# Optimization experiments

Hardware: AMD Instinct MI355X
Metric: run time of the kernel (lower is better)

Reference implementation:

```python
import jax, jax.numpy as jnp
import numpy as np

DIM = 1024
NH = 16        # query heads
NKV = 4        # kv heads
HD = 64        # head dim
GROUPS = NH // NKV
SPATIAL = 16
NZ = SPATIAL * SPATIAL  # 256 latent tokens with 2D structure
SOFT_CAP = 50.0
SCALE = HD ** -0.5
EPS = 1e-6


def rope_2d_cos_sin(nz, hd, spatial, dtype):
    # 2D RoPE: first half of head_dim encodes row position, second half column.
    pos = jnp.arange(nz)
    row = (pos // spatial).astype(jnp.float32)
    col = (pos % spatial).astype(jnp.float32)
    quarter = hd // 4
    inv_freq = 1.0 / (10000.0 ** (jnp.arange(quarter, dtype=jnp.float32) / quarter))
    f_row = row[:, None] * inv_freq[None, :]   # (nz, hd/4)
    f_col = col[:, None] * inv_freq[None, :]   # (nz, hd/4)
    emb = jnp.concatenate([f_row, f_col], axis=-1)      # (nz, hd/2)
    emb = jnp.concatenate([emb, emb], axis=-1)          # (nz, hd)
    return jnp.cos(emb).astype(dtype), jnp.sin(emb).astype(dtype)


def rotate_half(x):
    x1, x2 = jnp.split(x, 2, axis=-1)
    return jnp.concatenate([-x2, x1], axis=-1)


def apply_rotary(x, cos, sin):
    return x * cos + rotate_half(x) * sin


def rms_norm(x, w):
    # RMSNorm over head_dim with learned per-dim scale (QKNorm)
    return x * jax.lax.rsqrt(jnp.mean(x * x, axis=-1, keepdims=True) + EPS) * w


def setup_inputs() -> dict:
    key = jax.random.key(0)
    ks = jax.random.split(key, 7)
    B, T, S = 4, 16, 264
    x = jax.random.normal(ks[0], (B, T, S, DIM), dtype=jnp.float32)
    wq = jax.random.normal(ks[1], (NH * HD, DIM), dtype=jnp.float32) * 0.02
    wk = jax.random.normal(ks[2], (NKV * HD, DIM), dtype=jnp.float32) * 0.02
    wv = jax.random.normal(ks[3], (NKV * HD, DIM), dtype=jnp.float32) * 0.02
    wo = jax.random.normal(ks[4], (DIM, NH * HD), dtype=jnp.float32) * 0.02
    q_norm_w = jnp.ones((HD,), dtype=jnp.float32)
    k_norm_w = jnp.ones((HD,), dtype=jnp.float32)
    return {"x": x, "wq": wq, "wk": wk, "wv": wv, "wo": wo,
            "q_norm_w": q_norm_w, "k_norm_w": k_norm_w}


def reference(x, wq, wk, wv, wo, q_norm_w, k_norm_w):
    B, T, S, D = x.shape
    xf = x.reshape(B * T, S, D)
    # projections (torch Linear: y = x @ W.T)
    q = (xf @ wq.T).reshape(B * T, S, NH, HD).transpose(0, 2, 1, 3)   # (BT,NH,S,HD)
    k = (xf @ wk.T).reshape(B * T, S, NKV, HD).transpose(0, 2, 1, 3)  # (BT,NKV,S,HD)
    v = (xf @ wv.T).reshape(B * T, S, NKV, HD).transpose(0, 2, 1, 3)
    # QKNorm
    q = rms_norm(q, q_norm_w)
    k = rms_norm(k, k_norm_w)
    # partial 2D RoPE on latent tokens only
    cos, sin = rope_2d_cos_sin(NZ, HD, SPATIAL, q.dtype)
    cos = cos[None, None]  # (1,1,NZ,HD)
    sin = sin[None, None]
    q = jnp.concatenate([apply_rotary(q[:, :, :NZ], cos, sin), q[:, :, NZ:]], axis=2)
    k = jnp.concatenate([apply_rotary(k[:, :, :NZ], cos, sin), k[:, :, NZ:]], axis=2)
    # GQA: expand kv heads (repeat_interleave == jnp.repeat)
    k = jnp.repeat(k, GROUPS, axis=1)
    v = jnp.repeat(v, GROUPS, axis=1)
    # attention with soft cap
    attn = jnp.einsum("bhqd,bhkd->bhqk", q, k) * SCALE
    attn = SOFT_CAP * jnp.tanh(attn / SOFT_CAP)
    attn = jax.nn.softmax(attn, axis=-1)
    out = jnp.einsum("bhqk,bhkd->bhqd", attn, v)
    out = out.transpose(0, 2, 1, 3).reshape(B * T, S, NH * HD)
    out = out @ wo.T
    return out.reshape(B, T, S, D)
```

## Files before the change

kernel.cpp:

```cpp
#include <hip/hip_runtime.h>

typedef __bf16 bf16;
typedef __bf16 bf16x8 __attribute__((ext_vector_type(8)));
typedef float  f32x4  __attribute__((ext_vector_type(4)));

#define DIM   1024
#define NH    16
#define NKV   4
#define HD    64
#define SLEN  264
#define BTOT  64
#define MROWS (BTOT * SLEN)
#define NQKV  1536
#define NZ    256
#define VPAD  288

__device__ __forceinline__ void gl_lds16(const bf16* g, bf16* l) {
    __builtin_amdgcn_global_load_lds((__attribute__((address_space(1))) void*)(g),
                                     (__attribute__((address_space(3))) void*)(l),
                                     16, 0, 0);
}

__global__ void cvt_f32_bf16(const float* __restrict__ src, bf16* __restrict__ dst, int n) {
    int i = (blockIdx.x * 256 + threadIdx.x) * 4;
    if (i < n) {
        float4 v = *(const float4*)(src + i);
        dst[i + 0] = (bf16)v.x; dst[i + 1] = (bf16)v.y;
        dst[i + 2] = (bf16)v.z; dst[i + 3] = (bf16)v.w;
    }
}

__global__ void cvt_wcat(const float* __restrict__ wq, const float* __restrict__ wk,
                         const float* __restrict__ wv, bf16* __restrict__ dst) {
    int i = (blockIdx.x * 256 + threadIdx.x) * 4;
    const float* src; int off;
    if (i < 1024 * 1024)      { src = wq; off = i; }
    else if (i < 1280 * 1024) { src = wk; off = i - 1024 * 1024; }
    else                      { src = wv; off = i - 1280 * 1024; }
    float4 v = *(const float4*)(src + off);
    dst[i + 0] = (bf16)v.x; dst[i + 1] = (bf16)v.y;
    dst[i + 2] = (bf16)v.z; dst[i + 3] = (bf16)v.w;
}

__global__ void rope_tab_kernel(float2* __restrict__ ctab) {
    int i = blockIdx.x * 256 + threadIdx.x;
    int s = i >> 5, d = i & 31;
    const float LN1 = 0.5756462732485115f;
    float pos = (d < 16) ? (float)(s >> 4) : (float)(s & 15);
    float ang = pos * expf(-(float)(d & 15) * LN1);
    float sn, cs; sincosf(ang, &sn, &cs);
    ctab[i] = make_float2(cs, sn);
}

#define GEMM_STAGE_PTRS(Mptr, tileRow, K, P)                                   \
    const bf16* P[4];                                                          \
    {                                                                          \
        _Pragma("unroll")                                                      \
        for (int k = 0; k < 4; k++) {                                          \
            int s = k * 256 + tid;                                             \
            int r = s >> 3, cp = s & 7;                                        \
            int c = cp ^ (r & 7);                                              \
            P[k] = (Mptr) + (size_t)((tileRow) + r) * (K) + c * 8;             \
        }                                                                      \
    }

__device__ __forceinline__ int swz(int row, int chunk) {
    return row * 64 + ((chunk ^ (row & 7)) * 8);
}

__global__ __launch_bounds__(256) void gemm_qkv(const bf16* __restrict__ A,
                                                const bf16* __restrict__ Bw,
                                                bf16* __restrict__ out,
                                                const float* __restrict__ qw,
                                                const float* __restrict__ kw,
                                                const float2* __restrict__ ctab) {
    __shared__ __align__(16) bf16 As[128 * 64];
    __shared__ __align__(16) bf16 Bs[128 * 64];
    const int tid  = threadIdx.x;
    const int wid  = tid >> 6, lane = tid & 63;
    const int quad = lane >> 4, r16 = lane & 15;
    const int bid = blockIdx.x;
    const int g = bid / 48, rr = bid - g * 48;
    const int bm = g * 4 + (rr & 3), bn = rr >> 2;
    const int wm = wid & 1, wn = wid >> 1;

    GEMM_STAGE_PTRS(A,  bm * 128, DIM, Ap)
    GEMM_STAGE_PTRS(Bw, bn * 128, DIM, Bp)

    f32x4 acc[4][4];
#pragma unroll
    for (int i = 0; i < 4; i++)
#pragma unroll
        for (int j = 0; j < 4; j++) acc[i][j] = (f32x4){0.f, 0.f, 0.f, 0.f};

    for (int k0 = 0; k0 < DIM; k0 += 64) {
        __syncthreads();
#pragma unroll
        for (int k = 0; k < 4; k++) {
            gl_lds16(Ap[k] + k0, As + (k * 256 + wid * 64) * 8);
            gl_lds16(Bp[k] + k0, Bs + (k * 256 + wid * 64) * 8);
        }
        __syncthreads();
#pragma unroll
        for (int ks = 0; ks < 2; ks++) {
            bf16x8 a[4], b[4];
#pragma unroll
            for (int i = 0; i < 4; i++) {
                a[i] = *(const bf16x8*)&As[swz(wm * 64 + i * 16 + r16, ks * 4 + quad)];
                b[i] = *(const bf16x8*)&Bs[swz(wn * 64 + i * 16 + r16, ks * 4 + quad)];
            }
#pragma unroll
            for (int i = 0; i < 4; i++)
#pragma unroll
                for (int j = 0; j < 4; j++)
                    acc[i][j] = __builtin_amdgcn_mfma_f32_16x16x32_bf16(a[i], b[j], acc[i][j], 0, 0, 0);
        }
    }

    const int colbase = bn * 128 + wn * 64;
    const int rowbase = bm * 128 + wm * 64;
    if (bn < 10) {
        const float* w = (bn < 8) ? qw : kw;
        float wreg[4];
#pragma unroll
        for (int j = 0; j < 4; j++) wreg[j] = w[j * 16 + r16];
#pragma unroll
        for (int i = 0; i < 4; i++)
#pragma unroll
            for (int r = 0; r < 4; r++) {
                float ss = 0.f;
#pragma unroll
                for (int j = 0; j < 4; j++) ss += acc[i][j][r] * acc[i][j][r];
                ss += __shfl_xor(ss, 1, 64);
                ss += __shfl_xor(ss, 2, 64);
                ss += __shfl_xor(ss, 4, 64);
                ss += __shfl_xor(ss, 8, 64);
                float rms = rsqrtf(ss * (1.f / 64.f) + 1e-6f);
                float xv[4];
#pragma unroll
                for (int j = 0; j < 4; j++) xv[j] = acc[i][j][r] * rms * wreg[j];
                int gm = rowbase + i * 16 + quad * 4 + r;
                int s = gm % SLEN;
                if (s < NZ) {
                    float2 cs0 = ctab[s * 32 + r16];
                    float2 cs1 = ctab[s * 32 + 16 + r16];
                    float a0 = xv[0] * cs0.x - xv[2] * cs0.y;
                    float a2 = xv[2] * cs0.x + xv[0] * cs0.y;
                    float a1 = xv[1] * cs1.x - xv[3] * cs1.y;
                    float a3 = xv[3] * cs1.x + xv[1] * cs1.y;
                    xv[0] = a0; xv[1] = a1; xv[2] = a2; xv[3] = a3;
                }
                size_t rowoff = (size_t)gm * NQKV + colbase + r16;
#pragma unroll
                for (int j = 0; j < 4; j++) out[rowoff + j * 16] = (bf16)xv[j];
            }
    } else {
#pragma unroll
        for (int i = 0; i < 4; i++)
#pragma unroll
            for (int j = 0; j < 4; j++)
#pragma unroll
                for (int r = 0; r < 4; r++) {
                    int gm = rowbase + i * 16 + quad * 4 + r;
                    int gn = colbase + j * 16 + r16;
                    out[(size_t)gm * NQKV + gn] = (bf16)acc[i][j][r];
                }
    }
}

__global__ __launch_bounds__(256) void gemm_bt(const bf16* __restrict__ A,
                                               const bf16* __restrict__ Bw,
                                               float* __restrict__ Cout) {
    __shared__ __align__(16) bf16 As[128 * 64];
    __shared__ __align__(16) bf16 Bs[128 * 64];
    const int tid  = threadIdx.x;
    const int wid  = tid >> 6, lane = tid & 63;
    const int quad = lane >> 4, r16 = lane & 15;
    const int bid = blockIdx.x;
    const int g = bid / 32, rr = bid - g * 32;
    const int bm = g * 4 + (rr & 3), bn = rr >> 2;
    const int wm = wid & 1, wn = wid >> 1;

    GEMM_STAGE_PTRS(A,  bm * 128, DIM, Ap)
    GEMM_STAGE_PTRS(Bw, bn * 128, DIM, Bp)

    f32x4 acc[4][4];
#pragma unroll
    for (int i = 0; i < 4; i++)
#pragma unroll
        for (int j = 0; j < 4; j++) acc[i][j] = (f32x4){0.f, 0.f, 0.f, 0.f};

    for (int k0 = 0; k0 < DIM; k0 += 64) {
        __syncthreads();
#pragma unroll
        for (int k = 0; k < 4; k++) {
            gl_lds16(Ap[k] + k0, As + (k * 256 + wid * 64) * 8);
            gl_lds16(Bp[k] + k0, Bs + (k * 256 + wid * 64) * 8);
        }
        __syncthreads();
#pragma unroll
        for (int ks = 0; ks < 2; ks++) {
            bf16x8 a[4], b[4];
#pragma unroll
            for (int i = 0; i < 4; i++) {
                a[i] = *(const bf16x8*)&As[swz(wm * 64 + i * 16 + r16, ks * 4 + quad)];
                b[i] = *(const bf16x8*)&Bs[swz(wn * 64 + i * 16 + r16, ks * 4 + quad)];
            }
#pragma unroll
            for (int i = 0; i < 4; i++)
#pragma unroll
                for (int j = 0; j < 4; j++)
                    acc[i][j] = __builtin_amdgcn_mfma_f32_16x16x32_bf16(a[i], b[j], acc[i][j], 0, 0, 0);
        }
    }

#pragma unroll
    for (int i = 0; i < 4; i++)
#pragma unroll
        for (int j = 0; j < 4; j++)
#pragma unroll
            for (int r = 0; r < 4; r++) {
                int gm = bm * 128 + wm * 64 + i * 16 + quad * 4 + r;
                int gn = bn * 128 + wn * 64 + j * 16 + r16;
                Cout[(size_t)gm * DIM + gn] = acc[i][j][r];
            }
}

__global__ __launch_bounds__(256) void vtrans_kernel(const bf16* __restrict__ qkv,
                                                     bf16* __restrict__ vt) {
    __shared__ bf16 Ls[64 * 272];
    const int tid = threadIdx.x;
    const int b = blockIdx.x, bt = b >> 2, kv = b & 3;
    const int part = tid >> 5;
    const int rr   = tid & 31;
#pragma unroll
    for (int pass = 0; pass < 9; ++pass) {
        int row = pass * 32 + rr;
        if (row < SLEN) {
            bf16x8 v = *(const bf16x8*)(qkv + (size_t)(bt * SLEN + row) * NQKV + 1280 + kv * 64 + part * 8);
#pragma unroll
            for (int j = 0; j < 8; j++) Ls[(part * 8 + j) * 272 + row] = v[j];
        }
    }
    __syncthreads();
    const int d = tid >> 2, seg = tid & 3;
    size_t obase = ((size_t)b * 64 + d) * VPAD;
#pragma unroll
    for (int m = 0; m < 9; ++m) {
        int col = seg * 72 + m * 8;
        bf16x8 o;
#pragma unroll
        for (int j = 0; j < 8; j++) {
            int s = col + j;
            o[j] = (s < SLEN) ? Ls[d * 272 + s] : (bf16)0.f;
        }
        *(bf16x8*)(vt + obase + col) = o;
    }
}

__global__ __launch_bounds__(256) void attn_kernel(const bf16* __restrict__ qkv,
                                                   const bf16* __restrict__ vt,
                                                   bf16* __restrict__ aout) {
    const int PLD = 40;
    __shared__ __align__(16) bf16 Pb[4][2][16 * PLD];

    const int tid = threadIdx.x;
    const int wid = tid >> 6, lane = tid & 63;
    const int quad = lane >> 4, r16 = lane & 15;
    const int qp = blockIdx.x;
    const int kv = blockIdx.y, bt = blockIdx.z;
    const int h = kv * 4 + wid;

    bf16x8 qa[2][2];
#pragma unroll
    for (int qi = 0; qi < 2; qi++) {
        int q0 = qp * 32 + qi * 16 + r16;
        int qcl = q0 < SLEN ? q0 : SLEN - 1;
        const bf16* qb = qkv + (size_t)(bt * SLEN + qcl) * NQKV + h * HD + quad * 8;
        qa[qi][0] = *(const bf16x8*)qb;
        qa[qi][1] = *(const bf16x8*)(qb + 32);
    }

    f32x4 oacc[2][4];
    float lsum[2][4];
#pragma unroll
    for (int qi = 0; qi < 2; qi++)
#pragma unroll
        for (int i = 0; i < 4; i++) { oacc[qi][i] = (f32x4){0.f, 0.f, 0.f, 0.f}; lsum[qi][i] = 0.f; }

    const bf16* kbase = qkv + (size_t)bt * SLEN * NQKV + 1024 + kv * HD + quad * 8;
    const bf16* vbase = vt + (size_t)(bt * 4 + kv) * HD * VPAD;

    bf16x8 nk[2][2];
#pragma unroll
    for (int kt = 0; kt < 2; kt++) {
        int key = kt * 16 + r16;
        const bf16* kp = kbase + (size_t)key * NQKV;
        nk[kt][0] = *(const bf16x8*)kp;
        nk[kt][1] = *(const bf16x8*)(kp + 32);
    }

    for (int c = 0; c < 9; ++c) {
        bf16x8 ck[2][2];
#pragma unroll
        for (int kt = 0; kt < 2; kt++) { ck[kt][0] = nk[kt][0]; ck[kt][1] = nk[kt][1]; }
        if (c < 8) {
#pragma unroll
            for (int kt = 0; kt < 2; kt++) {
                int key = (c + 1) * 32 + kt * 16 + r16;
                int kc = key < SLEN ? key : SLEN - 1;
                const bf16* kp = kbase + (size_t)kc * NQKV;
                nk[kt][0] = *(const bf16x8*)kp;
                nk[kt][1] = *(const bf16x8*)(kp + 32);
            }
        }
        bf16x8 cv[4];
#pragma unroll
        for (int dt = 0; dt < 4; ++dt)
            cv[dt] = *(const bf16x8*)(vbase + (size_t)(dt * 16 + r16) * VPAD + c * 32 + quad * 8);

        f32x4 s[2][2];
#pragma unroll
        for (int qi = 0; qi < 2; qi++)
#pragma unroll
            for (int kt = 0; kt < 2; kt++) {
                f32x4 t = (f32x4){0.f, 0.f, 0.f, 0.f};
                t = __builtin_amdgcn_mfma_f32_16x16x32_bf16(qa[qi][0], ck[kt][0], t, 0, 0, 0);
                t = __builtin_amdgcn_mfma_f32_16x16x32_bf16(qa[qi][1], ck[kt][1], t, 0, 0, 0);
                s[qi][kt] = t;
            }

#pragma unroll
        for (int qi = 0; qi < 2; qi++) {
            bf16* Pw = &Pb[wid][qi][0];
#pragma unroll
            for (int kt = 0; kt < 2; kt++)
#pragma unroll
                for (int r = 0; r < 4; ++r) {
                    int key = c * 32 + kt * 16 + r16;
                    float sc = s[qi][kt][r];
                    float z = sc * 0.0025f;
                    float z2 = z * z;
                    float poly = fmaf(z2, fmaf(z2, 0.133333333f, -0.333333333f), 1.f);
                    float p = exp2f(sc * 0.18033688f * poly);
                    p = (key < SLEN) ? p : 0.f;
                    bf16 pb = (bf16)p;
                    lsum[qi][r] += (float)pb;
                    Pw[(quad * 4 + r) * PLD + kt * 16 + r16] = pb;
                }
            bf16x8 pa = *(const bf16x8*)&Pw[r16 * PLD + quad * 8];
#pragma unroll
            for (int dt = 0; dt < 4; ++dt)
                oacc[qi][dt] = __builtin_amdgcn_mfma_f32_16x16x32_bf16(pa, cv[dt], oacc[qi][dt], 0, 0, 0);
        }
    }

#pragma unroll
    for (int qi = 0; qi < 2; qi++)
#pragma unroll
        for (int r = 0; r < 4; ++r) {
            float l = lsum[qi][r];
            l += __shfl_xor(l, 1, 64);
            l += __shfl_xor(l, 2, 64);
            l += __shfl_xor(l, 4, 64);
            l += __shfl_xor(l, 8, 64);
            float inv = 1.f / l;
            int q = qp * 32 + qi * 16 + quad * 4 + r;
            if (q < SLEN) {
                size_t base = (size_t)(bt * SLEN + q) * (NH * HD) + h * HD;
#pragma unroll
                for (int dt = 0; dt < 4; ++dt)
                    aout[base + dt * 16 + r16] = (bf16)(oacc[qi][dt][r] * inv);
            }
        }
}

extern "C" void kernel_launch(void* const* d_in, const int* in_sizes, int n_in,
                              void* d_out, int out_size, void* d_ws, size_t ws_size,
                              hipStream_t stream) {
    const float* x   = (const float*)d_in[0];
    const float* wq  = (const float*)d_in[1];
    const float* wk  = (const float*)d_in[2];
    const float* wv  = (const float*)d_in[3];
    const float* wo  = (const float*)d_in[4];
    const float* qnw = (const float*)d_in[5];
    const float* knw = (const float*)d_in[6];

    bf16* xbf  = (bf16*)d_ws;
    bf16* wcat = xbf  + (size_t)MROWS * DIM;
    bf16* wobf = wcat + (size_t)NQKV * DIM;
    bf16* qkv  = wobf + (size_t)DIM * DIM;
    bf16* vt   = qkv  + (size_t)MROWS * NQKV;
    float2* ctab = (float2*)(vt + (size_t)BTOT * NKV * HD * VPAD);
    bf16* aout = xbf;

    rope_tab_kernel<<<32, 256, 0, stream>>>(ctab);
    cvt_f32_bf16<<<(MROWS * DIM) / 1024, 256, 0, stream>>>(x, xbf, MROWS * DIM);
    cvt_wcat<<<(NQKV * DIM) / 1024, 256, 0, stream>>>(wq, wk, wv, wcat);
    cvt_f32_bf16<<<(DIM * DIM) / 1024, 256, 0, stream>>>(wo, wobf, DIM * DIM);

    gemm_qkv<<<(MROWS / 128) * (NQKV / 128), 256, 0, stream>>>(xbf, wcat, qkv, qnw, knw, ctab);
    vtrans_kernel<<<BTOT * NKV, 256, 0, stream>>>(qkv, vt);
    attn_kernel<<<dim3(9, NKV, BTOT), 256, 0, stream>>>(qkv, vt, aout);
    gemm_bt<<<(MROWS / 128) * (DIM / 128), 256, 0, stream>>>(aout, wobf, (float*)d_out);
}
```

Before: 351.6 us.

## Rewrite projection GEMMs as 256x256 tiles with multi-buffered LDS pipeline

Both projection GEMMs now use a shared 256x256-tile core with 512 threads (8 waves). It stages A and B into four LDS buffers each, with an interleaved prefetch schedule, vmcnt gating, raised wave priority around the MFMA blocks, and an XCD-aware workgroup remap. The aim is to overlap global-to-LDS loads with MFMA work and raise arithmetic intensity per tile, in place of the old single-buffer 128x128 loop that synchronised twice per K step. The cost is more LDS per block and hand-tuned barrier ordering, and correctness depends on 264-row sequences mapping onto 256-row tiles, which the QKNorm/RoPE epilogue handles per row.

```diff
diff --git a/kernel.cpp b/kernel.cpp
--- a/kernel.cpp
+++ b/kernel.cpp
@@ -52,177 +52,209 @@
     ctab[i] = make_float2(cs, sn);
 }
 
-#define GEMM_STAGE_PTRS(Mptr, tileRow, K, P)                                   \
-    const bf16* P[4];                                                          \
-    {                                                                          \
-        _Pragma("unroll")                                                      \
-        for (int k = 0; k < 4; k++) {                                          \
-            int s = k * 256 + tid;                                             \
-            int r = s >> 3, cp = s & 7;                                        \
-            int c = cp ^ (r & 7);                                              \
-            P[k] = (Mptr) + (size_t)((tileRow) + r) * (K) + c * 8;             \
-        }                                                                      \
-    }
-
-__device__ __forceinline__ int swz(int row, int chunk) {
-    return row * 64 + ((chunk ^ (row & 7)) * 8);
-}
-
-__global__ __launch_bounds__(256) void gemm_qkv(const bf16* __restrict__ A,
+
+#define GATE4  asm volatile("s_waitcnt vmcnt(4)" ::: "memory")
+#define NOGATE do {} while (0)
+
+#define STAGE_A(DST, H, KT) do {                                                       \
+    gl_lds16(Ag + (size_t)((H) * 128 + ars[0]) * DIM + (KT) * 64 + acs[0] * 8,         \
+             (DST) + (wid * 64) * 8);                                                  \
+    gl_lds16(Ag + (size_t)((H) * 128 + ars[1]) * DIM + (KT) * 64 + acs[1] * 8,         \
+             (DST) + (512 + wid * 64) * 8);                                            \
+} while (0)
+
+#define STAGE_B(DST, KS, KT) do {                                                      \
+    gl_lds16(Bg + (size_t)brs[0] * DIM + (KT) * 64 + (KS) * 32 + bcs[0] * 8,           \
+             (DST) + (wid * 64) * 8);                                                  \
+    gl_lds16(Bg + (size_t)brs[1] * DIM + (KT) * 64 + (KS) * 32 + bcs[1] * 8,           \
+             (DST) + (512 + wid * 64) * 8);                                            \
+} while (0)
+
+#define PHASE(AARR, BARR, AA, KS, STAGE_STMT, GATE_STMT) do {                          \
+    const bf16* Ab_ = (AARR) + aRdBase + axor[KS];                                     \
+    const bf16* Bb_ = (BARR) + bRdBase + bxorv;                                        \
+    bf16x8 af_[4], bf_[4];                                                             \
+    _Pragma("unroll")                                                                  \
+    for (int i_ = 0; i_ < 4; i_++) af_[i_] = *(const bf16x8*)(Ab_ + i_ * 1024);        \
+    _Pragma("unroll")                                                                  \
+    for (int n_ = 0; n_ < 4; n_++) bf_[n_] = *(const bf16x8*)(Bb_ + n_ * 512);         \
+    STAGE_STMT;                                                                        \
+    GATE_STMT;                                                                         \
+    asm volatile("s_barrier" ::: "memory");                                            \
+    __builtin_amdgcn_s_setprio(1);                                                     \
+    _Pragma("unroll")                                                                  \
+    for (int i_ = 0; i_ < 4; i_++)                                                     \
+        _Pragma("unroll")                                                              \
+        for (int n_ = 0; n_ < 4; n_++)                                                 \
+            acc[AA][i_][n_] = __builtin_amdgcn_mfma_f32_16x16x32_bf16(                 \
+                af_[i_], bf_[n_], acc[AA][i_][n_], 0, 0, 0);                           \
+    __builtin_amdgcn_s_setprio(0);                                                     \
+    asm volatile("s_barrier" ::: "memory");                                            \
+} while (0)
+
+__device__ __forceinline__ void gemm256_core(const bf16* __restrict__ Ag,
+                                             const bf16* __restrict__ Bg,
+                                             f32x4 (&acc)[2][4][4]) {
+    __shared__ __align__(16) bf16 A00[128 * 64], A01[128 * 64], A10[128 * 64], A11[128 * 64];
+    __shared__ __align__(16) bf16 B00[256 * 32], B01[256 * 32], B10[256 * 32], B11[256 * 32];
+
+    const int tid  = threadIdx.x;
+    const int wid  = tid >> 6, lane = tid & 63;
+    const int quad = lane >> 4, r16 = lane & 15;
+    const int wm = wid & 1, wn = wid >> 1;
+
+    int ars[2], acs[2], brs[2], bcs[2];
+#pragma unroll
+    for (int k = 0; k < 2; k++) {
+        int s = k * 512 + tid;
+        ars[k] = s >> 3; acs[k] = (s & 7) ^ (ars[k] & 7);
+        brs[k] = s >> 2; bcs[k] = (s & 3) ^ (brs[k] & 3);
+    }
+    const int aRdBase = (wm * 64 + r16) * 64;
+    const int bRdBase = (wn * 64 + r16) * 32;
+    const int axor[2] = { (quad ^ (r16 & 7)) * 8, ((4 + quad) ^ (r16 & 7)) * 8 };
+    const int bxorv   = (quad ^ (r16 & 3)) * 8;
+
+    STAGE_A(A00, 0, 0); STAGE_A(A01, 1, 0);
+    STAGE_B(B00, 0, 0); STAGE_B(B01, 1, 0);
+    STAGE_A(A10, 0, 1); STAGE_B(B10, 0, 1);
+    GATE4;
+    asm volatile("s_barrier" ::: "memory");
+
+#pragma unroll 1
+    for (int it = 0; it < 8; ++it) {
+        const int t1 = 2 * it + 1;
+        int t2 = 2 * it + 2; if (t2 > 15) t2 = 15;
+        int t3 = 2 * it + 3; if (t3 > 15) t3 = 15;
+        PHASE(A00, B00, 0, 0, STAGE_A(A11, 1, t1), NOGATE);
+        PHASE(A00, B01, 0, 1, STAGE_B(B11, 1, t1), NOGATE);
+        PHASE(A01, B00, 1, 0, STAGE_A(A00, 0, t2), NOGATE);
+        PHASE(A01, B01, 1, 1, STAGE_B(B00, 0, t2), GATE4);
+        PHASE(A10, B10, 0, 0, STAGE_A(A01, 1, t2), NOGATE);
+        PHASE(A10, B11, 0, 1, STAGE_B(B01, 1, t2), NOGATE);
+        PHASE(A11, B10, 1, 0, STAGE_A(A10, 0, t3), NOGATE);
+        PHASE(A11, B11, 1, 1, STAGE_B(B10, 0, t3), GATE4);
+    }
+}
+
+__device__ __forceinline__ int xcd_swizzle(int orig, int nwg) {
+    int q = nwg >> 3, r = nwg & 7;
+    int xcd = orig & 7, lid = orig >> 3;
+    return (xcd < r ? xcd * (q + 1) : r * (q + 1) + (xcd - r) * q) + lid;
+}
+
+__global__ __launch_bounds__(512) void gemm_qkv(const bf16* __restrict__ A,
                                                 const bf16* __restrict__ Bw,
                                                 bf16* __restrict__ out,
                                                 const float* __restrict__ qw,
                                                 const float* __restrict__ kw,
                                                 const float2* __restrict__ ctab) {
-    __shared__ __align__(16) bf16 As[128 * 64];
-    __shared__ __align__(16) bf16 Bs[128 * 64];
+    const int nwg = (MROWS / 256) * (NQKV / 256);
+    int wg = xcd_swizzle(blockIdx.x, nwg);
+    const int bm = wg / 6, bn = wg - bm * 6;
+
+    f32x4 acc[2][4][4];
+#pragma unroll
+    for (int a = 0; a < 2; a++)
+#pragma unroll
+        for (int i = 0; i < 4; i++)
+#pragma unroll
+            for (int n = 0; n < 4; n++) acc[a][i][n] = (f32x4){0.f, 0.f, 0.f, 0.f};
+
+    gemm256_core(A + (size_t)bm * 256 * DIM, Bw + (size_t)bn * 256 * DIM, acc);
+
     const int tid  = threadIdx.x;
     const int wid  = tid >> 6, lane = tid & 63;
     const int quad = lane >> 4, r16 = lane & 15;
-    const int bid = blockIdx.x;
-    const int g = bid / 48, rr = bid - g * 48;
-    const int bm = g * 4 + (rr & 3), bn = rr >> 2;
     const int wm = wid & 1, wn = wid >> 1;
-
-    GEMM_STAGE_PTRS(A,  bm * 128, DIM, Ap)
-    GEMM_STAGE_PTRS(Bw, bn * 128, DIM, Bp)
-
-    f32x4 acc[4][4];
-#pragma unroll
-    for (int i = 0; i < 4; i++)
-#pragma unroll
-        for (int j = 0; j < 4; j++) acc[i][j] = (f32x4){0.f, 0.f, 0.f, 0.f};
-
-    for (int k0 = 0; k0 < DIM; k0 += 64) {
-        __syncthreads();
-#pragma unroll
-        for (int k = 0; k < 4; k++) {
-            gl_lds16(Ap[k] + k0, As + (k * 256 + wid * 64) * 8);
-            gl_lds16(Bp[k] + k0, Bs + (k * 256 + wid * 64) * 8);
-        }
-        __syncthreads();
-#pragma unroll
-        for (int ks = 0; ks < 2; ks++) {
-            bf16x8 a[4], b[4];
-#pragma unroll
-            for (int i = 0; i < 4; i++) {
-                a[i] = *(const bf16x8*)&As[swz(wm * 64 + i * 16 + r16, ks * 4 + quad)];
-                b[i] = *(const bf16x8*)&Bs[swz(wn * 64 + i * 16 + r16, ks * 4 + quad)];
-            }
+    const int colbase = bn * 256 + wn * 64;
+    const int rowb    = bm * 256 + wm * 64;
+
+    if (bn < 5) {
+        const float* w = (bn < 4) ? qw : kw;
+        float wreg[4];
+#pragma unroll
+        for (int n = 0; n < 4; n++) wreg[n] = w[n * 16 + r16];
+#pragma unroll
+        for (int a = 0; a < 2; a++)
 #pragma unroll
             for (int i = 0; i < 4; i++)
 #pragma unroll
-                for (int j = 0; j < 4; j++)
-                    acc[i][j] = __builtin_amdgcn_mfma_f32_16x16x32_bf16(a[i], b[j], acc[i][j], 0, 0, 0);
-        }
-    }
-
-    const int colbase = bn * 128 + wn * 64;
-    const int rowbase = bm * 128 + wm * 64;
-    if (bn < 10) {
-        const float* w = (bn < 8) ? qw : kw;
-        float wreg[4];
-#pragma unroll
-        for (int j = 0; j < 4; j++) wreg[j] = w[j * 16 + r16];
-#pragma unroll
-        for (int i = 0; i < 4; i++)
-#pragma unroll
-            for (int r = 0; r < 4; r++) {
-                float ss = 0.f;
-#pragma unroll
-                for (int j = 0; j < 4; j++) ss += acc[i][j][r] * acc[i][j][r];
-                ss += __shfl_xor(ss, 1, 64);
-                ss += __shfl_xor(ss, 2, 64);
-                ss += __shfl_xor(ss, 4, 64);
-                ss += __shfl_xor(ss, 8, 64);
-                float rms = rsqrtf(ss * (1.f / 64.f) + 1e-6f);
-                float xv[4];
-#pragma unroll
-                for (int j = 0; j < 4; j++) xv[j] = acc[i][j][r] * rms * wreg[j];
-                int gm = rowbase + i * 16 + quad * 4 + r;
-                int s = gm % SLEN;
-                if (s < NZ) {
-                    float2 cs0 = ctab[s * 32 + r16];
-                    float2 cs1 = ctab[s * 32 + 16 + r16];
-                    float a0 = xv[0] * cs0.x - xv[2] * cs0.y;
-                    float a2 = xv[2] * cs0.x + xv[0] * cs0.y;
-                    float a1 = xv[1] * cs1.x - xv[3] * cs1.y;
-                    float a3 = xv[3] * cs1.x + xv[1] * cs1.y;
-                    xv[0] = a0; xv[1] = a1; xv[2] = a2; xv[3] = a3;
+                for (int r = 0; r < 4; r++) {
+                    float ss = 0.f;
+#pragma unroll
+                    for (int n = 0; n < 4; n++) ss += acc[a][i][n][r] * acc[a][i][n][r];
+                    ss += __shfl_xor(ss, 1, 64);
+                    ss += __shfl_xor(ss, 2, 64);
+                    ss += __shfl_xor(ss, 4, 64);
+                    ss += __shfl_xor(ss, 8, 64);
+                    float rms = rsqrtf(ss * (1.f / 64.f) + 1e-6f);
+                    float xv[4];
+#pragma unroll
+                    for (int n = 0; n < 4; n++) xv[n] = acc[a][i][n][r] * rms * wreg[n];
+                    int gm = rowb + a * 128 + i * 16 + quad * 4 + r;
+                    int s = gm % SLEN;
+                    if (s < NZ) {
+                        float2 cs0 = ctab[s * 32 + r16];
+                        float2 cs1 = ctab[s * 32 + 16 + r16];
+                        float a0 = xv[0] * cs0.x - xv[2] * cs0.y;
+                        float a2 = xv[2] * cs0.x + xv[0] * cs0.y;
+                        float a1 = xv[1] * cs1.x - xv[3] * cs1.y;
+                        float a3 = xv[3] * cs1.x + xv[1] * cs1.y;
+                        xv[0] = a0; xv[1] = a1; xv[2] = a2; xv[3] = a3;
+                    }
+                    size_t rowoff = (size_t)gm * NQKV + colbase + r16;
+#pragma unroll
+                    for (int n = 0; n < 4; n++) out[rowoff + n * 16] = (bf16)xv[n];
                 }
-                size_t rowoff = (size_t)gm * NQKV + colbase + r16;
-#pragma unroll
-                for (int j = 0; j < 4; j++) out[rowoff + j * 16] = (bf16)xv[j];
-            }
     } else {
 #pragma unroll
-        for (int i = 0; i < 4; i++)
-#pragma unroll
-            for (int j = 0; j < 4; j++)
+        for (int a = 0; a < 2; a++)
+#pragma unroll
+            for (int i = 0; i < 4; i++)
 #pragma unroll
                 for (int r = 0; r < 4; r++) {
-                    int gm = rowbase + i * 16 + quad * 4 + r;
-                    int gn = colbase + j * 16 + r16;
-                    out[(size_t)gm * NQKV + gn] = (bf16)acc[i][j][r];
+                    int gm = rowb + a * 128 + i * 16 + quad * 4 + r;
+                    size_t rowoff = (size_t)gm * NQKV + colbase + r16;
+#pragma unroll
+                    for (int n = 0; n < 4; n++) out[rowoff + n * 16] = (bf16)acc[a][i][n][r];
                 }
     }
 }
 
-__global__ __launch_bounds__(256) void gemm_bt(const bf16* __restrict__ A,
+__global__ __launch_bounds__(512) void gemm_bt(const bf16* __restrict__ A,
                                                const bf16* __restrict__ Bw,
                                                float* __restrict__ Cout) {
-    __shared__ __align__(16) bf16 As[128 * 64];
-    __shared__ __align__(16) bf16 Bs[128 * 64];
+    const int nwg = (MROWS / 256) * (DIM / 256);
+    int wg = xcd_swizzle(blockIdx.x, nwg);
+    const int bm = wg / 4, bn = wg - bm * 4;
+
+    f32x4 acc[2][4][4];
+#pragma unroll
+    for (int a = 0; a < 2; a++)
+#pragma unroll
+        for (int i = 0; i < 4; i++)
+#pragma unroll
+            for (int n = 0; n < 4; n++) acc[a][i][n] = (f32x4){0.f, 0.f, 0.f, 0.f};
+
+    gemm256_core(A + (size_t)bm * 256 * DIM, Bw + (size_t)bn * 256 * DIM, acc);
+
     const int tid  = threadIdx.x;
     const int wid  = tid >> 6, lane = tid & 63;
     const int quad = lane >> 4, r16 = lane & 15;
-    const int bid = blockIdx.x;
-    const int g = bid / 32, rr = bid - g * 32;
-    const int bm = g * 4 + (rr & 3), bn = rr >> 2;
     const int wm = wid & 1, wn = wid >> 1;
-
-    GEMM_STAGE_PTRS(A,  bm * 128, DIM, Ap)
-    GEMM_STAGE_PTRS(Bw, bn * 128, DIM, Bp)
-
-    f32x4 acc[4][4];
-#pragma unroll
-    for (int i = 0; i < 4; i++)
-#pragma unroll
-        for (int j = 0; j < 4; j++) acc[i][j] = (f32x4){0.f, 0.f, 0.f, 0.f};
-
-    for (int k0 = 0; k0 < DIM; k0 += 64) {
-        __syncthreads();
-#pragma unroll
-        for (int k = 0; k < 4; k++) {
-            gl_lds16(Ap[k] + k0, As + (k * 256 + wid * 64) * 8);
-            gl_lds16(Bp[k] + k0, Bs + (k * 256 + wid * 64) * 8);
-        }
-        __syncthreads();
-#pragma unroll
-        for (int ks = 0; ks < 2; ks++) {
-            bf16x8 a[4], b[4];
-#pragma unroll
-            for (int i = 0; i < 4; i++) {
-                a[i] = *(const bf16x8*)&As[swz(wm * 64 + i * 16 + r16, ks * 4 + quad)];
-                b[i] = *(const bf16x8*)&Bs[swz(wn * 64 + i * 16 + r16, ks * 4 + quad)];
-            }
-#pragma unroll
-            for (int i = 0; i < 4; i++)
-#pragma unroll
-                for (int j = 0; j < 4; j++)
-                    acc[i][j] = __builtin_amdgcn_mfma_f32_16x16x32_bf16(a[i], b[j], acc[i][j], 0, 0, 0);
-        }
-    }
-
-#pragma unroll
-    for (int i = 0; i < 4; i++)
-#pragma unroll
-        for (int j = 0; j < 4; j++)
+    const int colbase = bn * 256 + wn * 64;
+    const int rowb    = bm * 256 + wm * 64;
+#pragma unroll
+    for (int a = 0; a < 2; a++)
+#pragma unroll
+        for (int i = 0; i < 4; i++)
 #pragma unroll
             for (int r = 0; r < 4; r++) {
-                int gm = bm * 128 + wm * 64 + i * 16 + quad * 4 + r;
-                int gn = bn * 128 + wn * 64 + j * 16 + r16;
-                Cout[(size_t)gm * DIM + gn] = acc[i][j][r];
+                int gm = rowb + a * 128 + i * 16 + quad * 4 + r;
+                size_t rowoff = (size_t)gm * DIM + colbase + r16;
+#pragma unroll
+                for (int n = 0; n < 4; n++) Cout[rowoff + n * 16] = acc[a][i][n][r];
             }
 }
 
@@ -399,8 +431,8 @@
     cvt_wcat<<<(NQKV * DIM) / 1024, 256, 0, stream>>>(wq, wk, wv, wcat);
     cvt_f32_bf16<<<(DIM * DIM) / 1024, 256, 0, stream>>>(wo, wobf, DIM * DIM);
 
-    gemm_qkv<<<(MROWS / 128) * (NQKV / 128), 256, 0, stream>>>(xbf, wcat, qkv, qnw, knw, ctab);
+    gemm_qkv<<<(MROWS / 256) * (NQKV / 256), 512, 0, stream>>>(xbf, wcat, qkv, qnw, knw, ctab);
     vtrans_kernel<<<BTOT * NKV, 256, 0, stream>>>(qkv, vt);
     attn_kernel<<<dim3(9, NKV, BTOT), 256, 0, stream>>>(qkv, vt, aout);
-    gemm_bt<<<(MROWS / 128) * (DIM / 128), 256, 0, stream>>>(aout, wobf, (float*)d_out);
-}
+    gemm_bt<<<(MROWS / 256) * (DIM / 256), 512, 0, stream>>>(aout, wobf, (float*)d_out);
+}
```

After: 372.0 us. +5.8%, slower.

## Rewrite QKV GEMM as 256x256 tile, 8-wave pipelined kernel with XCD swizzle

Applied to the files above, without the earlier changes.

Replaces the 128x128, 4-wave QKV projection GEMM with a 256x256 tile, 512-thread kernel. It double-buffers quarter tiles in LDS and overlaps global-to-LDS loads with MFMA phases through explicit vmcnt gating, barriers and setprio. Blocks are remapped so neighbouring tiles land on the same XCD, which should improve L2 reuse. The aim is higher MFMA utilisation and fewer sync stalls, at the cost of 128KB of LDS per block, only one block per CU, and a smaller grid (396 blocks), which may hurt load balance.

```diff
diff --git a/kernel.cpp b/kernel.cpp
--- a/kernel.cpp
+++ b/kernel.cpp
@@ -52,6 +52,170 @@
     ctab[i] = make_float2(cs, sn);
 }
 
+__device__ __forceinline__ int xcd_swizzle(int orig, int nwg) {
+    int q = nwg >> 3, r = nwg & 7;
+    int xcd = orig & 7, lid = orig >> 3;
+    return (xcd < r ? xcd * (q + 1) : r * (q + 1) + (xcd - r) * q) + lid;
+}
+
+
+#define GATE2  asm volatile("s_waitcnt vmcnt(2)" ::: "memory")
+#define NOGATE do {} while (0)
+
+#define STAGE(DST, G, H, KT) do {                                              \
+    gl_lds16((G) + (size_t)((H) * 128 + rs0) * DIM + (KT) * 64 + cs0 * 8,      \
+             (DST) + wid * 512);                                               \
+    gl_lds16((G) + (size_t)((H) * 128 + 64 + rs0) * DIM + (KT) * 64 + cs0 * 8, \
+             (DST) + 4096 + wid * 512);                                        \
+} while (0)
+
+#define PHASE(Ad, Bd, AA, KS, STAGE_STMT, GATE_STMT) do {                      \
+    bf16x8 af_[4], bf_[4];                                                     \
+    _Pragma("unroll")                                                          \
+    for (int i_ = 0; i_ < 4; i_++) {                                           \
+        af_[i_] = *(const bf16x8*)((Ad) + aRdBase + i_ * 1024 + xorv[KS]);     \
+        bf_[i_] = *(const bf16x8*)((Bd) + bRdBase + i_ * 1024 + xorv[KS]);     \
+    }                                                                          \
+    STAGE_STMT;                                                                \
+    GATE_STMT;                                                                 \
+    __builtin_amdgcn_s_barrier();                                              \
+    asm volatile("s_waitcnt lgkmcnt(0)" ::: "memory");                         \
+    __builtin_amdgcn_sched_barrier(0);                                         \
+    __builtin_amdgcn_s_setprio(1);                                             \
+    _Pragma("unroll")                                                          \
+    for (int i_ = 0; i_ < 4; i_++)                                             \
+        _Pragma("unroll")                                                      \
+        for (int n_ = 0; n_ < 4; n_++)                                         \
+            acc[AA][i_][n_] = __builtin_amdgcn_mfma_f32_16x16x32_bf16(         \
+                af_[i_], bf_[n_], acc[AA][i_][n_], 0, 0, 0);                   \
+    __builtin_amdgcn_s_setprio(0);                                             \
+    __builtin_amdgcn_s_barrier();                                              \
+} while (0)
+
+__device__ __forceinline__ void gemm256_core(const bf16* __restrict__ Ag,
+                                             const bf16* __restrict__ Bg,
+                                             f32x4 (&acc)[2][4][4]) {
+    __shared__ __align__(16) bf16 A00[128 * 64], A01[128 * 64], A10[128 * 64], A11[128 * 64];
+    __shared__ __align__(16) bf16 B00[128 * 64], B01[128 * 64], B10[128 * 64], B11[128 * 64];
+
+    const int tid  = threadIdx.x;
+    const int wid  = tid >> 6, lane = tid & 63;
+    const int quad = lane >> 4, r16 = lane & 15;
+    const int wm = wid & 1, wn = wid >> 1;
+
+    const int rs0 = tid >> 3;
+    const int cs0 = (tid & 7) ^ (rs0 & 7);
+
+    const int aRdBase = (wm * 64 + r16) * 64;
+    const int bRdBase = ((wn & 1) * 64 + r16) * 64;
+    const int xorv[2] = { (quad ^ (r16 & 7)) * 8, ((4 + quad) ^ (r16 & 7)) * 8 };
+
+    const bf16* Bd0 = (wn & 2) ? B01 : B00;
+    const bf16* Bd1 = (wn & 2) ? B11 : B10;
+
+    STAGE(A00, Ag, 0, 0);
+    STAGE(A01, Ag, 1, 0);
+    STAGE(B00, Bg, 0, 0);
+    STAGE(B01, Bg, 1, 0);
+    STAGE(A10, Ag, 0, 1);
+    GATE2;
+    __builtin_amdgcn_s_barrier();
+
+#pragma unroll 1
+    for (int it = 0; it < 8; ++it) {
+        const int t1 = 2 * it + 1;
+        int t2 = 2 * it + 2; if (t2 > 15) t2 = 15;
+        int t3 = 2 * it + 3; if (t3 > 15) t3 = 15;
+        PHASE(A00, Bd0, 0, 0, STAGE(A11, Ag, 1, t1), NOGATE);
+        PHASE(A00, Bd0, 0, 1, STAGE(B10, Bg, 0, t1), NOGATE);
+        PHASE(A01, Bd0, 1, 0, STAGE(B11, Bg, 1, t1), NOGATE);
+        PHASE(A01, Bd0, 1, 1, STAGE(A00, Ag, 0, t2), GATE2);
+        PHASE(A10, Bd1, 0, 0, STAGE(A01, Ag, 1, t2), NOGATE);
+        PHASE(A10, Bd1, 0, 1, STAGE(B00, Bg, 0, t2), NOGATE);
+        PHASE(A11, Bd1, 1, 0, STAGE(B01, Bg, 1, t2), NOGATE);
+        PHASE(A11, Bd1, 1, 1, STAGE(A10, Ag, 0, t3), GATE2);
+    }
+}
+
+__global__ __launch_bounds__(512) void gemm_qkv(const bf16* __restrict__ A,
+                                                const bf16* __restrict__ Bw,
+                                                bf16* __restrict__ out,
+                                                const float* __restrict__ qw,
+                                                const float* __restrict__ kw,
+                                                const float2* __restrict__ ctab) {
+    const int nwg = (MROWS / 256) * (NQKV / 256);
+    int wg = xcd_swizzle(blockIdx.x, nwg);
+    const int bm = wg / 6, bn = wg - bm * 6;
+
+    f32x4 acc[2][4][4];
+#pragma unroll
+    for (int a = 0; a < 2; a++)
+#pragma unroll
+        for (int i = 0; i < 4; i++)
+#pragma unroll
+            for (int n = 0; n < 4; n++) acc[a][i][n] = (f32x4){0.f, 0.f, 0.f, 0.f};
+
+    gemm256_core(A + (size_t)bm * 256 * DIM, Bw + (size_t)bn * 256 * DIM, acc);
+
+    const int tid  = threadIdx.x;
+    const int wid  = tid >> 6, lane = tid & 63;
+    const int quad = lane >> 4, r16 = lane & 15;
+    const int wm = wid & 1, wn = wid >> 1;
+    const int colbase = bn * 256 + wn * 64;
+    const int rowb    = bm * 256 + wm * 64;
+
+    if (bn < 5) {
+        const float* w = (bn < 4) ? qw : kw;
+        float wreg[4];
+#pragma unroll
+        for (int n = 0; n < 4; n++) wreg[n] = w[n * 16 + r16];
+#pragma unroll
+        for (int a = 0; a < 2; a++)
+#pragma unroll
+            for (int i = 0; i < 4; i++)
+#pragma unroll
+                for (int r = 0; r < 4; r++) {
+                    float ss = 0.f;
+#pragma unroll
+                    for (int n = 0; n < 4; n++) ss += acc[a][i][n][r] * acc[a][i][n][r];
+                    ss += __shfl_xor(ss, 1, 64);
+                    ss += __shfl_xor(ss, 2, 64);
+                    ss += __shfl_xor(ss, 4, 64);
+                    ss += __shfl_xor(ss, 8, 64);
+                    float rms = rsqrtf(ss * (1.f / 64.f) + 1e-6f);
+                    float xv[4];
+#pragma unroll
+                    for (int n = 0; n < 4; n++) xv[n] = acc[a][i][n][r] * rms * wreg[n];
+                    int gm = rowb + a * 128 + i * 16 + quad * 4 + r;
+                    int s = gm % SLEN;
+                    if (s < NZ) {
+                        float2 cs0 = ctab[s * 32 + r16];
+                        float2 cs1 = ctab[s * 32 + 16 + r16];
+                        float a0 = xv[0] * cs0.x - xv[2] * cs0.y;
+                        float a2 = xv[2] * cs0.x + xv[0] * cs0.y;
+                        float a1 = xv[1] * cs1.x - xv[3] * cs1.y;
+                        float a3 = xv[3] * cs1.x + xv[1] * cs1.y;
+                        xv[0] = a0; xv[1] = a1; xv[2] = a2; xv[3] = a3;
+                    }
+                    size_t rowoff = (size_t)gm * NQKV + colbase + r16;
+#pragma unroll
+                    for (int n = 0; n < 4; n++) out[rowoff + n * 16] = (bf16)xv[n];
+                }
+    } else {
+#pragma unroll
+        for (int a = 0; a < 2; a++)
+#pragma unroll
+            for (int i = 0; i < 4; i++)
+#pragma unroll
+                for (int r = 0; r < 4; r++) {
+                    int gm = rowb + a * 128 + i * 16 + quad * 4 + r;
+                    size_t rowoff = (size_t)gm * NQKV + colbase + r16;
+#pragma unroll
+                    for (int n = 0; n < 4; n++) out[rowoff + n * 16] = (bf16)acc[a][i][n][r];
+                }
+    }
+}
+
 #define GEMM_STAGE_PTRS(Mptr, tileRow, K, P)                                   \
     const bf16* P[4];                                                          \
     {                                                                          \
@@ -66,106 +230,6 @@
 
 __device__ __forceinline__ int swz(int row, int chunk) {
     return row * 64 + ((chunk ^ (row & 7)) * 8);
-}
-
-__global__ __launch_bounds__(256) void gemm_qkv(const bf16* __restrict__ A,
-                                                const bf16* __restrict__ Bw,
-                                                bf16* __restrict__ out,
-                                                const float* __restrict__ qw,
-                                                const float* __restrict__ kw,
-                                                const float2* __restrict__ ctab) {
-    __shared__ __align__(16) bf16 As[128 * 64];
-    __shared__ __align__(16) bf16 Bs[128 * 64];
-    const int tid  = threadIdx.x;
-    const int wid  = tid >> 6, lane = tid & 63;
-    const int quad = lane >> 4, r16 = lane & 15;
-    const int bid = blockIdx.x;
-    const int g = bid / 48, rr = bid - g * 48;
-    const int bm = g * 4 + (rr & 3), bn = rr >> 2;
-    const int wm = wid & 1, wn = wid >> 1;
-
-    GEMM_STAGE_PTRS(A,  bm * 128, DIM, Ap)
-    GEMM_STAGE_PTRS(Bw, bn * 128, DIM, Bp)
-
-    f32x4 acc[4][4];
-#pragma unroll
-    for (int i = 0; i < 4; i++)
-#pragma unroll
-        for (int j = 0; j < 4; j++) acc[i][j] = (f32x4){0.f, 0.f, 0.f, 0.f};
-
-    for (int k0 = 0; k0 < DIM; k0 += 64) {
-        __syncthreads();
-#pragma unroll
-        for (int k = 0; k < 4; k++) {
-            gl_lds16(Ap[k] + k0, As + (k * 256 + wid * 64) * 8);
-            gl_lds16(Bp[k] + k0, Bs + (k * 256 + wid * 64) * 8);
-        }
-        __syncthreads();
-#pragma unroll
-        for (int ks = 0; ks < 2; ks++) {
-            bf16x8 a[4], b[4];
-#pragma unroll
-            for (int i = 0; i < 4; i++) {
-                a[i] = *(const bf16x8*)&As[swz(wm * 64 + i * 16 + r16, ks * 4 + quad)];
-                b[i] = *(const bf16x8*)&Bs[swz(wn * 64 + i * 16 + r16, ks * 4 + quad)];
-            }
-#pragma unroll
-            for (int i = 0; i < 4; i++)
-#pragma unroll
-                for (int j = 0; j < 4; j++)
-                    acc[i][j] = __builtin_amdgcn_mfma_f32_16x16x32_bf16(a[i], b[j], acc[i][j], 0, 0, 0);
-        }
-    }
-
-    const int colbase = bn * 128 + wn * 64;
-    const int rowbase = bm * 128 + wm * 64;
-    if (bn < 10) {
-        const float* w = (bn < 8) ? qw : kw;
-        float wreg[4];
-#pragma unroll
-        for (int j = 0; j < 4; j++) wreg[j] = w[j * 16 + r16];
-#pragma unroll
-        for (int i = 0; i < 4; i++)
-#pragma unroll
-            for (int r = 0; r < 4; r++) {
-                float ss = 0.f;
-#pragma unroll
-                for (int j = 0; j < 4; j++) ss += acc[i][j][r] * acc[i][j][r];
-                ss += __shfl_xor(ss, 1, 64);
-                ss += __shfl_xor(ss, 2, 64);
-                ss += __shfl_xor(ss, 4, 64);
-                ss += __shfl_xor(ss, 8, 64);
-                float rms = rsqrtf(ss * (1.f / 64.f) + 1e-6f);
-                float xv[4];
-#pragma unroll
-                for (int j = 0; j < 4; j++) xv[j] = acc[i][j][r] * rms * wreg[j];
-                int gm = rowbase + i * 16 + quad * 4 + r;
-                int s = gm % SLEN;
-                if (s < NZ) {
-                    float2 cs0 = ctab[s * 32 + r16];
-                    float2 cs1 = ctab[s * 32 + 16 + r16];
-                    float a0 = xv[0] * cs0.x - xv[2] * cs0.y;
-                    float a2 = xv[2] * cs0.x + xv[0] * cs0.y;
-                    float a1 = xv[1] * cs1.x - xv[3] * cs1.y;
-                    float a3 = xv[3] * cs1.x + xv[1] * cs1.y;
-                    xv[0] = a0; xv[1] = a1; xv[2] = a2; xv[3] = a3;
-                }
-                size_t rowoff = (size_t)gm * NQKV + colbase + r16;
-#pragma unroll
-                for (int j = 0; j < 4; j++) out[rowoff + j * 16] = (bf16)xv[j];
-            }
-    } else {
-#pragma unroll
-        for (int i = 0; i < 4; i++)
-#pragma unroll
-            for (int j = 0; j < 4; j++)
-#pragma unroll
-                for (int r = 0; r < 4; r++) {
-                    int gm = rowbase + i * 16 + quad * 4 + r;
-                    int gn = colbase + j * 16 + r16;
-                    out[(size_t)gm * NQKV + gn] = (bf16)acc[i][j][r];
-                }
-    }
 }
 
 __global__ __launch_bounds__(256) void gemm_bt(const bf16* __restrict__ A,
@@ -399,7 +463,7 @@
     cvt_wcat<<<(NQKV * DIM) / 1024, 256, 0, stream>>>(wq, wk, wv, wcat);
     cvt_f32_bf16<<<(DIM * DIM) / 1024, 256, 0, stream>>>(wo, wobf, DIM * DIM);
 
-    gemm_qkv<<<(MROWS / 128) * (NQKV / 128), 256, 0, stream>>>(xbf, wcat, qkv, qnw, knw, ctab);
+    gemm_qkv<<<(MROWS / 256) * (NQKV / 256), 512, 0, stream>>>(xbf, wcat, qkv, qnw, knw, ctab);
     vtrans_kernel<<<BTOT * NKV, 256, 0, stream>>>(qkv, vt);
     attn_kernel<<<dim3(9, NKV, BTOT), 256, 0, stream>>>(qkv, vt, aout);
     gemm_bt<<<(MROWS / 128) * (DIM / 128), 256, 0, stream>>>(aout, wobf, (float*)d_out);
```

Result: no change. 344.8 us (-1.9%).
